# Performance work log

Measured on AMD Instinct MI355X. Metric: run time of the kernel, lower is better.

Reference implementation:

```python
import jax, jax.numpy as jnp
import numpy as np

N = 50000      # nodes
E = 800000     # edges (before self loops)
IN = 61        # input node features
H = 256        # hidden
HEADS = 8
C = H // HEADS # per-head channels = 32
L = 4          # GAT layers
EPS = 1e-5


def setup_inputs() -> dict:
    key = jax.random.key(0)
    ks = jax.random.split(key, 10)
    s = 0.05
    return {
        "x": jax.random.normal(ks[0], (N, IN), jnp.float32),
        "edge_index": jax.random.randint(ks[1], (2, E), 0, N),
        "in_W": jax.random.normal(ks[2], (IN, H), jnp.float32) * s,
        "in_b": jnp.zeros((H,), jnp.float32),
        "in_gamma": jnp.ones((H,), jnp.float32),
        "in_beta": jnp.zeros((H,), jnp.float32),
        "Ws": jax.random.normal(ks[3], (L, H, H), jnp.float32) * s,
        "att_src": jax.random.normal(ks[4], (L, HEADS, C), jnp.float32) * s,
        "att_dst": jax.random.normal(ks[5], (L, HEADS, C), jnp.float32) * s,
        "conv_b": jnp.zeros((L, H), jnp.float32),
        "bn_gamma": jnp.ones((L, H), jnp.float32),
        "bn_beta": jnp.zeros((L, H), jnp.float32),
        "mean_W": jax.random.normal(ks[6], (H, 1), jnp.float32) * s,
        "mean_b": jnp.zeros((1,), jnp.float32),
        "lv_W": jax.random.normal(ks[7], (H, 1), jnp.float32) * s,
        "lv_b": jnp.zeros((1,), jnp.float32),
    }


def _bn(h, gamma, beta):
    # training-mode BatchNorm1d: batch stats, biased variance
    mu = h.mean(axis=0)
    var = jnp.var(h, axis=0)
    return (h - mu) * jax.lax.rsqrt(var + EPS) * gamma + beta


def _gat_layer(h, src, dst, W, a_src, a_dst, bias):
    # h: [N,H] -> z: [N,HEADS,C]
    z = (h @ W).reshape(N, HEADS, C)
    e_src = jnp.einsum('nhc,hc->nh', z, a_src)  # [N,HEADS]
    e_dst = jnp.einsum('nhc,hc->nh', z, a_dst)
    e = jax.nn.leaky_relu(e_src[src] + e_dst[dst], 0.2)  # [Etot,HEADS]
    # segment softmax over destination neighborhoods
    emax = jax.ops.segment_max(e, dst, num_segments=N)
    p = jnp.exp(e - emax[dst])
    denom = jax.ops.segment_sum(p, dst, num_segments=N)
    alpha = p / denom[dst]
    # weighted scatter-aggregate of per-edge messages
    out = jax.ops.segment_sum(z[src] * alpha[:, :, None], dst, num_segments=N)
    return out.reshape(N, H) + bias


def reference(x, edge_index, in_W, in_b, in_gamma, in_beta, Ws, att_src,
              att_dst, conv_b, bn_gamma, bn_beta, mean_W, mean_b, lv_W, lv_b):
    loops = jnp.arange(N, dtype=edge_index.dtype)
    src = jnp.concatenate([edge_index[0], loops])  # add_self_loops=True
    dst = jnp.concatenate([edge_index[1], loops])
    # input projection: Linear -> BN -> ReLU (dropout off, deterministic)
    h = jax.nn.relu(_bn(x @ in_W + in_b, in_gamma, in_beta))
    for i in range(L):
        res = h
        h = _gat_layer(h, src, dst, Ws[i], att_src[i], att_dst[i], conv_b[i])
        h = jax.nn.relu(_bn(h, bn_gamma[i], bn_beta[i])) + res
    mean = (h @ mean_W + mean_b)[:, 0]
    log_var = jnp.clip((h @ lv_W + lv_b)[:, 0], -10.0, 10.0)
    return (mean, log_var)
```

## Files before the change

### kernel.cpp

```cpp
#include <hip/hip_runtime.h>
#include <hip/hip_fp16.h>

#define NN 50000
#define EE 800000
#define ETOT 850000
#define KIN 61
#define HH 256
#define NH 8
#define CC 32
#define LL 4
#define SCAN_NBLK 49

typedef __attribute__((ext_vector_type(8))) short bf16x8;
typedef __attribute__((ext_vector_type(4))) float f32x4;

__device__ __forceinline__ unsigned short f2b(float f) {
    unsigned u = __builtin_bit_cast(unsigned, f);
    u += 0x7fffu + ((u >> 16) & 1u);
    return (unsigned short)(u >> 16);
}
__device__ __forceinline__ float b2f(unsigned short h) {
    unsigned u = ((unsigned)h) << 16;
    return __builtin_bit_cast(float, u);
}
__device__ __forceinline__ unsigned short f2h(float f) {
    __half h = __float2half(f);
    return __builtin_bit_cast(unsigned short, h);
}
__device__ __forceinline__ float h2f(unsigned short u) {
    return __half2float(__builtin_bit_cast(__half, u));
}

__device__ __forceinline__ void gload16(const void* g, void* l) {
    __builtin_amdgcn_global_load_lds(
        (const __attribute__((address_space(1))) void*)g,
        (__attribute__((address_space(3))) void*)l, 16, 0, 0);
}


__global__ __launch_bounds__(256) void edge_hist(const int* __restrict__ ei,
                                                 int* __restrict__ counts) {
    int e = blockIdx.x * 256 + threadIdx.x;
    if (e >= ETOT) return;
    int d = (e < EE) ? ei[EE + e] : (e - EE);
    atomicAdd(&counts[d], 1);
}

__global__ __launch_bounds__(256) void scan1(const int* __restrict__ counts,
                                             int* __restrict__ tmp,
                                             int* __restrict__ bsums) {
    __shared__ int lds[256];
    int b = blockIdx.x, t = threadIdx.x;
    int base = b * 1024 + t * 4;
    int v0 = 0, v1 = 0, v2 = 0, v3 = 0;
    if (base + 0 < NN) v0 = counts[base + 0];
    if (base + 1 < NN) v1 = counts[base + 1];
    if (base + 2 < NN) v2 = counts[base + 2];
    if (base + 3 < NN) v3 = counts[base + 3];
    int s = v0 + v1 + v2 + v3;
    lds[t] = s;
    __syncthreads();
    for (int off = 1; off < 256; off <<= 1) {
        int x = (t >= off) ? lds[t - off] : 0;
        __syncthreads();
        lds[t] += x;
        __syncthreads();
    }
    int run = lds[t] - s;
    if (t == 255) bsums[b] = lds[255];
    run += v0; if (base + 0 < NN) tmp[base + 0] = run;
    run += v1; if (base + 1 < NN) tmp[base + 1] = run;
    run += v2; if (base + 2 < NN) tmp[base + 2] = run;
    run += v3; if (base + 3 < NN) tmp[base + 3] = run;
}

__global__ void scan2(int* __restrict__ bsums) {
    if (threadIdx.x == 0) {
        int acc = 0;
        for (int i = 0; i < SCAN_NBLK; ++i) { int t = bsums[i]; bsums[i] = acc; acc += t; }
    }
}

__global__ __launch_bounds__(256) void scan3(const int* __restrict__ tmp,
                                             const int* __restrict__ bsums,
                                             const int* __restrict__ counts,
                                             int* __restrict__ rowptr,
                                             int* __restrict__ cursor) {
    int i = blockIdx.x * 256 + threadIdx.x;
    if (i >= NN) return;
    int incl = tmp[i] + bsums[i >> 10];
    rowptr[i + 1] = incl;
    cursor[i] = incl - counts[i];
    if (i == 0) rowptr[0] = 0;
}

__global__ __launch_bounds__(256) void edge_scatter(const int* __restrict__ ei,
                                                    int* __restrict__ cursor,
                                                    int* __restrict__ ssrc) {
    int e = blockIdx.x * 256 + threadIdx.x;
    if (e >= ETOT) return;
    int s, d;
    if (e < EE) { s = ei[e]; d = ei[EE + e]; } else { s = d = e - EE; }
    int pos = atomicAdd(&cursor[d], 1);
    ssrc[pos] = s;
}

__global__ __launch_bounds__(256) void sort_rows(const int* __restrict__ rowptr,
                                                 int* __restrict__ ssrc) {
    int wid = (blockIdx.x * 256 + threadIdx.x) >> 6;
    int lane = threadIdx.x & 63;
    if (wid >= NN) return;
    int beg = rowptr[wid], end = rowptr[wid + 1];
    int L = end - beg;
    if (L > 64) return;
    int v = (lane < L) ? ssrc[beg + lane] : 0x7fffffff;
#pragma unroll
    for (int k = 2; k <= 64; k <<= 1) {
#pragma unroll
        for (int j = k >> 1; j > 0; j >>= 1) {
            int partner = __shfl_xor(v, j);
            bool up = ((lane & k) == 0);
            bool keepMin = (up == ((lane & j) == 0));
            int mn = min(v, partner), mx = max(v, partner);
            v = keepMin ? mn : mx;
        }
    }
    if (lane < L) ssrc[beg + lane] = v;
}


__global__ __launch_bounds__(256) void prep_wt(const float* __restrict__ Ws,
                                               unsigned short* __restrict__ WT) {
    int t = blockIdx.x * 256 + threadIdx.x;
    if (t >= LL * HH * HH) return;
    int l = t >> 16, rem = t & 65535;
    int n = rem >> 8, k = rem & 255;
    WT[t] = f2b(Ws[l * 65536 + k * HH + n]);
}

__global__ __launch_bounds__(256) void prep_inwt(const float* __restrict__ in_W,
                                                 unsigned short* __restrict__ WT) {
    int t = blockIdx.x * 256 + threadIdx.x;
    if (t >= HH * 64) return;
    int n = t >> 6, k = t & 63;
    WT[t] = (k < KIN) ? f2b(in_W[k * HH + n]) : 0;
}

__global__ __launch_bounds__(256) void prep_x(const float* __restrict__ x,
                                              unsigned short* __restrict__ xb) {
    int t = blockIdx.x * 256 + threadIdx.x;
    if (t >= NN * 64) return;
    int n = t >> 6, c = t & 63;
    xb[t] = (c < KIN) ? f2b(x[n * KIN + c]) : 0;
}

template<int ZHM>
__global__ __launch_bounds__(512) void gemm_mfma(const unsigned short* __restrict__ A,
                                                 const unsigned short* __restrict__ Bt,
                                                 unsigned short* __restrict__ C,
                                                 const float* __restrict__ asl,
                                                 const float* __restrict__ adl,
                                                 float* __restrict__ esrcT,
                                                 float* __restrict__ edstT,
                                                 int M, int K) {
    __shared__ unsigned short As[128 * 64];
    __shared__ unsigned short Bs[256 * 64];
    int row0 = blockIdx.x * 128;
    int tid = threadIdx.x;
    int w = tid >> 6, l = tid & 63;
    int wm = w >> 2, wn = w & 3;
    int r15 = l & 15, q = l >> 4;

    f32x4 acc[4][4] = {};

    int crow = l >> 3;
    int cs   = l & 7;

    for (int kt = 0; kt < K; kt += 64) {
        if (kt) __syncthreads();
#pragma unroll
        for (int c = 0; c < 2; ++c) {
            int r = w * 16 + c * 8 + crow;
            int sg = cs ^ (r & 7);
            int ga = row0 + r; if (ga >= M) ga = M - 1;
            gload16(&A[(size_t)ga * K + kt + sg * 8], &As[(w * 16 + c * 8) * 64]);
        }
#pragma unroll
        for (int c = 0; c < 4; ++c) {
            int r = w * 32 + c * 8 + crow;
            int sg = cs ^ (r & 7);
            gload16(&Bt[(size_t)r * K + kt + sg * 8], &Bs[(w * 32 + c * 8) * 64]);
        }
        __syncthreads();
#pragma unroll
        for (int kk = 0; kk < 2; ++kk) {
            bf16x8 aF[4], bF[4];
#pragma unroll
            for (int i = 0; i < 4; ++i) {
                int ar = wm * 64 + i * 16 + r15;
                aF[i] = *(bf16x8*)&As[ar * 64 + ((kk * 4 + q) ^ (ar & 7)) * 8];
                int br = wn * 64 + i * 16 + r15;
                bF[i] = *(bf16x8*)&Bs[br * 64 + ((kk * 4 + q) ^ (br & 7)) * 8];
            }
#pragma unroll
            for (int i = 0; i < 4; ++i)
#pragma unroll
                for (int j = 0; j < 4; ++j)
                    acc[i][j] = __builtin_amdgcn_mfma_f32_16x16x32_bf16(aF[i], bF[j], acc[i][j], 0, 0, 0);
        }
    }

#pragma unroll
    for (int i = 0; i < 4; ++i)
#pragma unroll
        for (int j = 0; j < 4; ++j) {
            int nc = wn * 64 + j * 16 + r15;
#pragma unroll
            for (int r = 0; r < 4; ++r) {
                int gr = row0 + wm * 64 + i * 16 + q * 4 + r;
                if (gr < M) {
                    if (ZHM)
                        C[(size_t)(nc >> 5) * NN * CC + (size_t)gr * CC + (nc & 31)] = f2h(acc[i][j][r]);
                    else
                        C[(size_t)gr * HH + nc] = f2b(acc[i][j][r]);
                }
            }
        }

    if constexpr (ZHM) {
        int hdbase = wn * 2;
        float as_[4], ad_[4];
#pragma unroll
        for (int j = 0; j < 4; ++j) {
            int idx = (hdbase + (j >> 1)) * CC + (j & 1) * 16 + r15;
            as_[j] = asl[idx];
            ad_[j] = adl[idx];
        }
#pragma unroll
        for (int h = 0; h < 2; ++h) {
#pragma unroll
            for (int i = 0; i < 4; ++i) {
                float pes[4], ped[4];
#pragma unroll
                for (int r = 0; r < 4; ++r) {
                    float v0 = h2f(f2h(acc[i][2 * h][r]));
                    float v1 = h2f(f2h(acc[i][2 * h + 1][r]));
                    pes[r] = v0 * as_[2 * h] + v1 * as_[2 * h + 1];
                    ped[r] = v0 * ad_[2 * h] + v1 * ad_[2 * h + 1];
                }
#pragma unroll
                for (int off = 1; off <= 8; off <<= 1) {
#pragma unroll
                    for (int r = 0; r < 4; ++r) {
                        pes[r] += __shfl_xor(pes[r], off);
                        ped[r] += __shfl_xor(ped[r], off);
                    }
                }
                int hd = hdbase + h;
                if (r15 < 8) {
                    int r = r15 & 3;
                    int gr = row0 + wm * 64 + i * 16 + q * 4 + r;
                    if (gr < M) {
                        if (r15 < 4) esrcT[(size_t)hd * NN + gr] = pes[r];
                        else         edstT[(size_t)hd * NN + gr] = ped[r];
                    }
                }
            }
        }
    }
}

#define MAXEB 2048
__global__ __launch_bounds__(256) void aggregate(const int* __restrict__ rowptr,
                                                 const int* __restrict__ ssrc,
                                                 const float* __restrict__ esrcT,
                                                 const float* __restrict__ edstT,
                                                 const unsigned short* __restrict__ zT,
                                                 unsigned short* __restrict__ outb,
                                                 float* __restrict__ sums) {
    __shared__ int   s_lds[MAXEB];
    __shared__ float p_lds[MAXEB];
    __shared__ int   rp_lds[33];
    __shared__ float ed_lds[32];
    __shared__ float ws1[4][8][4], ws2[4][8][4];
    int bid = blockIdx.x;
    int hd = bid & 7;
    int n0 = (bid >> 3) * 32;
    int tid = threadIdx.x;
    const float* esp = esrcT + (size_t)hd * NN;
    const unsigned short* zp = zT + (size_t)hd * NN * CC;

    if (tid <= 32) {
        int idx = n0 + tid;
        rp_lds[tid] = rowptr[idx > NN ? NN : idx];
    }
    if (tid < 32) {
        int nn = n0 + tid;
        ed_lds[tid] = (nn < NN) ? edstT[(size_t)hd * NN + nn] : 0.f;
    }
    __syncthreads();
    int beg0 = rp_lds[0];
    int total = rp_lds[32] - beg0;
    bool staged = (total <= MAXEB);
    if (staged) {
        for (int j = tid; j < total; j += 256) {
            int s = ssrc[beg0 + j];
            int jj = beg0 + j;
            int lo = 0, hi = 32;
#pragma unroll
            for (int st = 0; st < 5; ++st) {
                int mid = (lo + hi) >> 1;
                bool le = (rp_lds[mid] <= jj);
                lo = le ? mid : lo;
                hi = le ? hi : mid;
            }
            float e = esp[s] + ed_lds[lo];
            e = (e > 0.f) ? e : 0.2f * e;
            s_lds[j] = s;
            p_lds[j] = __expf(e);
        }
    }
    __syncthreads();

    int lane = tid & 63;
    int wv = tid >> 6;
    int g = lane >> 3;
    int nl = wv * 8 + g;
    int n = n0 + nl;
    int col = (lane & 7) * 4;
    bool act = n < NN;
    int jbeg = rp_lds[nl] - beg0;
    int jend = rp_lds[nl + 1] - beg0;

    float d0 = 0.f, d1 = 0.f, d2 = 0.f, d3 = 0.f;
    __half2 zero2 = __float2half2_rn(0.f);
    __half2 c0l = zero2, c0h = zero2, c1l = zero2, c1h = zero2;
    __half2 c2l = zero2, c2h = zero2, c3l = zero2, c3h = zero2;
    int j = jbeg;
    if (staged) {
        for (; j + 3 < jend; j += 4) {
            int s0 = s_lds[j], s1 = s_lds[j + 1], s2 = s_lds[j + 2], s3 = s_lds[j + 3];
            float p0 = p_lds[j], p1 = p_lds[j + 1], p2 = p_lds[j + 2], p3 = p_lds[j + 3];
            uint2 z0 = *(const uint2*)&zp[(size_t)(s0 * CC + col)];
            uint2 z1 = *(const uint2*)&zp[(size_t)(s1 * CC + col)];
            uint2 z2 = *(const uint2*)&zp[(size_t)(s2 * CC + col)];
            uint2 z3 = *(const uint2*)&zp[(size_t)(s3 * CC + col)];
            __half2 ph0 = __float2half2_rn(p0 * 0.0625f);
            __half2 ph1 = __float2half2_rn(p1 * 0.0625f);
            __half2 ph2 = __float2half2_rn(p2 * 0.0625f);
            __half2 ph3 = __float2half2_rn(p3 * 0.0625f);
            d0 += p0; d1 += p1; d2 += p2; d3 += p3;
            c0l = __hfma2(ph0, __builtin_bit_cast(__half2, z0.x), c0l);
            c0h = __hfma2(ph0, __builtin_bit_cast(__half2, z0.y), c0h);
            c1l = __hfma2(ph1, __builtin_bit_cast(__half2, z1.x), c1l);
            c1h = __hfma2(ph1, __builtin_bit_cast(__half2, z1.y), c1h);
            c2l = __hfma2(ph2, __builtin_bit_cast(__half2, z2.x), c2l);
            c2h = __hfma2(ph2, __builtin_bit_cast(__half2, z2.y), c2h);
            c3l = __hfma2(ph3, __builtin_bit_cast(__half2, z3.x), c3l);
            c3h = __hfma2(ph3, __builtin_bit_cast(__half2, z3.y), c3h);
        }
        for (; j < jend; ++j) {
            int s0 = s_lds[j];
            float p0 = p_lds[j];
            uint2 z0 = *(const uint2*)&zp[(size_t)(s0 * CC + col)];
            __half2 ph0 = __float2half2_rn(p0 * 0.0625f);
            d0 += p0;
            c0l = __hfma2(ph0, __builtin_bit_cast(__half2, z0.x), c0l);
            c0h = __hfma2(ph0, __builtin_bit_cast(__half2, z0.y), c0h);
        }
    } else {
        float ed = act ? ed_lds[nl] : 0.f;
        for (; j < jend; ++j) {
            int s0 = ssrc[beg0 + j];
            float es0 = esp[s0];
            uint2 z0 = *(const uint2*)&zp[(size_t)(s0 * CC + col)];
            float e0 = es0 + ed; e0 = (e0 > 0.f) ? e0 : 0.2f * e0;
            float p0 = __expf(e0);
            __half2 ph0 = __float2half2_rn(p0 * 0.0625f);
            d0 += p0;
            c0l = __hfma2(ph0, __builtin_bit_cast(__half2, z0.x), c0l);
            c0h = __hfma2(ph0, __builtin_bit_cast(__half2, z0.y), c0h);
        }
    }
    float v0 = 0.f, v1 = 0.f, v2 = 0.f, v3 = 0.f;
    if (act) {
        float den = (d0 + d1) + (d2 + d3);
        float inv = 16.f / den;
        float2 f0l = __half22float2(c0l), f1l = __half22float2(c1l);
        float2 f2l = __half22float2(c2l), f3l = __half22float2(c3l);
        float2 f0h = __half22float2(c0h), f1h = __half22float2(c1h);
        float2 f2h_ = __half22float2(c2h), f3h = __half22float2(c3h);
        ushort4 o;
        o.x = f2b(((f0l.x + f1l.x) + (f2l.x + f3l.x)) * inv);
        o.y = f2b(((f0l.y + f1l.y) + (f2l.y + f3l.y)) * inv);
        o.z = f2b(((f0h.x + f1h.x) + (f2h_.x + f3h.x)) * inv);
        o.w = f2b(((f0h.y + f1h.y) + (f2h_.y + f3h.y)) * inv);
        *(ushort4*)&outb[(size_t)n * HH + hd * CC + col] = o;
        v0 = b2f(o.x); v1 = b2f(o.y); v2 = b2f(o.z); v3 = b2f(o.w);
    }
    float q0 = v0 * v0, q1 = v1 * v1, q2 = v2 * v2, q3 = v3 * v3;
#pragma unroll
    for (int off = 8; off <= 32; off <<= 1) {
        v0 += __shfl_xor(v0, off); v1 += __shfl_xor(v1, off);
        v2 += __shfl_xor(v2, off); v3 += __shfl_xor(v3, off);
        q0 += __shfl_xor(q0, off); q1 += __shfl_xor(q1, off);
        q2 += __shfl_xor(q2, off); q3 += __shfl_xor(q3, off);
    }
    if (g == 0) {
        int slot = lane & 7;
        ws1[wv][slot][0] = v0; ws1[wv][slot][1] = v1;
        ws1[wv][slot][2] = v2; ws1[wv][slot][3] = v3;
        ws2[wv][slot][0] = q0; ws2[wv][slot][1] = q1;
        ws2[wv][slot][2] = q2; ws2[wv][slot][3] = q3;
    }
    __syncthreads();
    if (tid < 32) {
        int slot = tid & 7, k = tid >> 3;
        float s1v = ws1[0][slot][k] + ws1[1][slot][k] + ws1[2][slot][k] + ws1[3][slot][k];
        float s2v = ws2[0][slot][k] + ws2[1][slot][k] + ws2[2][slot][k] + ws2[3][slot][k];
        int ch = hd * CC + slot * 4 + k;
        atomicAdd(&sums[ch], s1v);
        atomicAdd(&sums[HH + ch], s2v);
    }
}

__global__ __launch_bounds__(256) void col_stats(const unsigned short* __restrict__ X,
                                                 float* __restrict__ sums) {
    int c = threadIdx.x;
    int rows_per_block = (NN + gridDim.x - 1) / gridDim.x;
    int r0 = blockIdx.x * rows_per_block;
    int r1 = min(NN, r0 + rows_per_block);
    float s = 0.f, q = 0.f;
    for (int r = r0; r < r1; ++r) {
        float v = b2f(X[(size_t)r * HH + c]);
        s += v; q += v * v;
    }
    atomicAdd(&sums[c], s);
    atomicAdd(&sums[HH + c], q);
}

__global__ __launch_bounds__(256) void bn_relu_add(const unsigned short* __restrict__ X,
                                                   const float* __restrict__ sums,
                                                   const float* __restrict__ gamma,
                                                   const float* __restrict__ beta,
                                                   const unsigned short* __restrict__ res,
                                                   unsigned short* __restrict__ outb) {
    int i = blockIdx.x * 256 + threadIdx.x;
    if (i >= NN * 64) return;
    int c4 = (i & 63) * 4;
    const float invN = 1.f / NN;
    ushort4 u = *(const ushort4*)(X + (size_t)i * 4);
    float v0 = b2f(u.x), v1 = b2f(u.y), v2 = b2f(u.z), v3 = b2f(u.w);
    float4 s1 = *(const float4*)&sums[c4];
    float4 s2 = *(const float4*)&sums[HH + c4];
    float4 gm = *(const float4*)&gamma[c4];
    float4 bt = *(const float4*)&beta[c4];
    float mn0 = s1.x * invN, mn1 = s1.y * invN, mn2 = s1.z * invN, mn3 = s1.w * invN;
    float rs0 = rsqrtf(fmaxf(s2.x * invN - mn0 * mn0, 0.f) + 1e-5f);
    float rs1 = rsqrtf(fmaxf(s2.y * invN - mn1 * mn1, 0.f) + 1e-5f);
    float rs2 = rsqrtf(fmaxf(s2.z * invN - mn2 * mn2, 0.f) + 1e-5f);
    float rs3 = rsqrtf(fmaxf(s2.w * invN - mn3 * mn3, 0.f) + 1e-5f);
    float r0 = fmaxf((v0 - mn0) * rs0 * gm.x + bt.x, 0.f);
    float r1 = fmaxf((v1 - mn1) * rs1 * gm.y + bt.y, 0.f);
    float r2 = fmaxf((v2 - mn2) * rs2 * gm.z + bt.z, 0.f);
    float r3 = fmaxf((v3 - mn3) * rs3 * gm.w + bt.w, 0.f);
    if (res) {
        ushort4 rv = *(const ushort4*)(res + (size_t)i * 4);
        r0 += b2f(rv.x); r1 += b2f(rv.y); r2 += b2f(rv.z); r3 += b2f(rv.w);
    }
    ushort4 ob;
    ob.x = f2b(r0); ob.y = f2b(r1); ob.z = f2b(r2); ob.w = f2b(r3);
    *(ushort4*)(outb + (size_t)i * 4) = ob;
}

__global__ __launch_bounds__(256) void out_proj(const unsigned short* __restrict__ h,
                                                const float* __restrict__ mW,
                                                const float* __restrict__ mb,
                                                const float* __restrict__ lW,
                                                const float* __restrict__ lb,
                                                float* __restrict__ out) {
    int wid = (blockIdx.x * 256 + threadIdx.x) >> 6;
    int lane = threadIdx.x & 63;
    if (wid >= NN) return;
    ushort4 hv = *(const ushort4*)&h[(size_t)wid * HH + lane * 4];
    float h0 = b2f(hv.x), h1 = b2f(hv.y), h2 = b2f(hv.z), h3 = b2f(hv.w);
    float4 wv = *(const float4*)&mW[lane * 4];
    float4 lv = *(const float4*)&lW[lane * 4];
    float sm = h0 * wv.x + h1 * wv.y + h2 * wv.z + h3 * wv.w;
    float sl = h0 * lv.x + h1 * lv.y + h2 * lv.z + h3 * lv.w;
    for (int off = 32; off > 0; off >>= 1) {
        sm += __shfl_down(sm, off);
        sl += __shfl_down(sl, off);
    }
    if (lane == 0) {
        out[wid] = sm + mb[0];
        float l = sl + lb[0];
        out[NN + wid] = fminf(10.f, fmaxf(-10.f, l));
    }
}

extern "C" void kernel_launch(void* const* d_in, const int* in_sizes, int n_in,
                              void* d_out, int out_size, void* d_ws, size_t ws_size,
                              hipStream_t stream) {
    const float* x        = (const float*)d_in[0];
    const int*   ei       = (const int*)d_in[1];
    const float* in_W     = (const float*)d_in[2];
    const float* in_gamma = (const float*)d_in[4];
    const float* in_beta  = (const float*)d_in[5];
    const float* Ws       = (const float*)d_in[6];
    const float* att_src  = (const float*)d_in[7];
    const float* att_dst  = (const float*)d_in[8];
    const float* bn_gamma = (const float*)d_in[10];
    const float* bn_beta  = (const float*)d_in[11];
    const float* mean_W   = (const float*)d_in[12];
    const float* mean_b   = (const float*)d_in[13];
    const float* lv_W     = (const float*)d_in[14];
    const float* lv_b     = (const float*)d_in[15];
    float* out = (float*)d_out;

    char* p = (char*)d_ws;
    unsigned short* z    = (unsigned short*)p; p += (size_t)NN * HH * 2;
    unsigned short* hb   = (unsigned short*)p; p += (size_t)NN * HH * 2;
    unsigned short* aggb = (unsigned short*)p; p += (size_t)NN * HH * 2;
    float* esrcT = (float*)p;                  p += (size_t)NN * NH * 4;
    float* edstT = (float*)p;                  p += (size_t)NN * NH * 4;
    float* sums = (float*)p;                   p += 512 * 4;
    unsigned short* WT   = (unsigned short*)p; p += (size_t)LL * HH * HH * 2;
    unsigned short* inWT = (unsigned short*)p; p += (size_t)HH * 64 * 2;
    int* counts = (int*)p;                     p += (size_t)NN * 4;
    int* rowptr = (int*)p;                     p += (size_t)(NN + 1) * 4;
    int* cursor = (int*)p;                     p += (size_t)NN * 4;
    int* ssrc   = (int*)p;                     p += (size_t)ETOT * 4;
    int* bsums  = (int*)p;                     p += 64 * 4;
    unsigned short* xb = aggb;

    hipMemsetAsync(counts, 0, NN * sizeof(int), stream);
    edge_hist<<<(ETOT + 255) / 256, 256, 0, stream>>>(ei, counts);
    scan1<<<SCAN_NBLK, 256, 0, stream>>>(counts, cursor, bsums);
    scan2<<<1, 64, 0, stream>>>(bsums);
    scan3<<<(NN + 255) / 256, 256, 0, stream>>>(cursor, bsums, counts, rowptr, cursor);
    edge_scatter<<<(ETOT + 255) / 256, 256, 0, stream>>>(ei, cursor, ssrc);
    sort_rows<<<(NN * 64 + 255) / 256, 256, 0, stream>>>(rowptr, ssrc);

    prep_wt<<<(LL * HH * HH + 255) / 256, 256, 0, stream>>>(Ws, WT);
    prep_inwt<<<(HH * 64 + 255) / 256, 256, 0, stream>>>(in_W, inWT);
    prep_x<<<(NN * 64 + 255) / 256, 256, 0, stream>>>(x, xb);

    gemm_mfma<0><<<(NN + 127) / 128, 512, 0, stream>>>(xb, inWT, z, nullptr, nullptr,
                                                       nullptr, nullptr, NN, 64);
    hipMemsetAsync(sums, 0, 512 * sizeof(float), stream);
    col_stats<<<1024, 256, 0, stream>>>(z, sums);
    bn_relu_add<<<(NN * 64 + 255) / 256, 256, 0, stream>>>(z, sums, in_gamma, in_beta,
                                                           nullptr, hb);

    for (int l = 0; l < LL; ++l) {
        const unsigned short* WTl = WT + (size_t)l * HH * HH;
        const float* asl = att_src + (size_t)l * NH * CC;
        const float* adl = att_dst + (size_t)l * NH * CC;
        const float* gl  = bn_gamma + (size_t)l * HH;
        const float* bl  = bn_beta + (size_t)l * HH;

        gemm_mfma<1><<<(NN + 127) / 128, 512, 0, stream>>>(hb, WTl, z, asl, adl,
                                                           esrcT, edstT, NN, HH);
        hipMemsetAsync(sums, 0, 512 * sizeof(float), stream);
        aggregate<<<((NN + 31) / 32) * 8, 256, 0, stream>>>(rowptr, ssrc, esrcT, edstT,
                                                            z, aggb, sums);
        bn_relu_add<<<(NN * 64 + 255) / 256, 256, 0, stream>>>(aggb, sums, gl, bl, hb, hb);
    }

    out_proj<<<(NN * 64 + 255) / 256, 256, 0, stream>>>(hb, mean_W, mean_b, lv_W, lv_b, out);
}
```

Baseline: 690.2 us.

## Fuse BatchNorm+ReLU+residual into GEMM A-load and final BN into output projection

Removes the standalone bn_relu_add kernels. Each layer's GEMM now computes the BN scale and shift from the column sums in shared memory. It applies BN, ReLU and the residual while staging the A tile, and writes the new hidden state as a side effect. The last layer's BN and residual are folded into the output-projection kernel. This saves a full read/write pass and a launch per layer, but the A tile is now loaded through registers with ALU work instead of async direct-to-LDS loads, which may slow the GEMM main loop.

```diff
diff --git a/kernel.cpp b/kernel.cpp
--- a/kernel.cpp
+++ b/kernel.cpp
@@ -26,9 +26,6 @@
 __device__ __forceinline__ unsigned short f2h(float f) {
     __half h = __float2half(f);
     return __builtin_bit_cast(unsigned short, h);
-}
-__device__ __forceinline__ float h2f(unsigned short u) {
-    return __half2float(__builtin_bit_cast(__half, u));
 }
 
 __device__ __forceinline__ void gload16(const void* g, void* l) {
@@ -154,23 +151,42 @@
     xb[t] = (c < KIN) ? f2b(x[n * KIN + c]) : 0;
 }
 
-template<int ZHM>
-__global__ __launch_bounds__(512) void gemm_mfma(const unsigned short* __restrict__ A,
+template<int MODE>
+__global__ __launch_bounds__(512) void gemm_mfma(const unsigned short* __restrict__ Asrc,
                                                  const unsigned short* __restrict__ Bt,
                                                  unsigned short* __restrict__ C,
                                                  const float* __restrict__ asl,
                                                  const float* __restrict__ adl,
                                                  float* __restrict__ esrcT,
                                                  float* __restrict__ edstT,
+                                                 const float* __restrict__ sums,
+                                                 const float* __restrict__ gamma,
+                                                 const float* __restrict__ beta,
+                                                 const unsigned short* __restrict__ res,
+                                                 unsigned short* __restrict__ hbNew,
                                                  int M, int K) {
     __shared__ unsigned short As[128 * 64];
     __shared__ unsigned short Bs[256 * 64];
+    __shared__ float scaleS[256], shiftS[256];
     int row0 = blockIdx.x * 128;
     int tid = threadIdx.x;
     int w = tid >> 6, l = tid & 63;
     int wm = w >> 2, wn = w & 3;
     int r15 = l & 15, q = l >> 4;
 
+    if constexpr (MODE == 1) {
+        if (tid < 256) {
+            const float invN = 1.f / NN;
+            float mn = sums[tid] * invN;
+            float var = fmaxf(sums[256 + tid] * invN - mn * mn, 0.f);
+            float rs = rsqrtf(var + 1e-5f);
+            float sc = rs * gamma[tid];
+            scaleS[tid] = sc;
+            shiftS[tid] = beta[tid] - mn * sc;
+        }
+        __syncthreads();
+    }
+
     f32x4 acc[4][4] = {};
 
     int crow = l >> 3;
@@ -182,8 +198,47 @@
         for (int c = 0; c < 2; ++c) {
             int r = w * 16 + c * 8 + crow;
             int sg = cs ^ (r & 7);
-            int ga = row0 + r; if (ga >= M) ga = M - 1;
-            gload16(&A[(size_t)ga * K + kt + sg * 8], &As[(w * 16 + c * 8) * 64]);
+            int ga = row0 + r;
+            if constexpr (MODE == 0) {
+                if (ga >= M) ga = M - 1;
+                gload16(&Asrc[(size_t)ga * K + kt + sg * 8], &As[(w * 16 + c * 8) * 64]);
+            } else {
+                unsigned short* dst = &As[(w * 16 + c * 8) * 64 + l * 8];
+                if (ga < M) {
+                    int ch = kt + sg * 8;
+                    ushort4 xlo = *(const ushort4*)&Asrc[(size_t)ga * 256 + ch];
+                    ushort4 xhi = *(const ushort4*)&Asrc[(size_t)ga * 256 + ch + 4];
+                    float4 sc0 = *(const float4*)&scaleS[ch];
+                    float4 sc1 = *(const float4*)&scaleS[ch + 4];
+                    float4 sh0 = *(const float4*)&shiftS[ch];
+                    float4 sh1 = *(const float4*)&shiftS[ch + 4];
+                    float f0 = fmaxf(b2f(xlo.x) * sc0.x + sh0.x, 0.f);
+                    float f1 = fmaxf(b2f(xlo.y) * sc0.y + sh0.y, 0.f);
+                    float f2 = fmaxf(b2f(xlo.z) * sc0.z + sh0.z, 0.f);
+                    float f3 = fmaxf(b2f(xlo.w) * sc0.w + sh0.w, 0.f);
+                    float f4 = fmaxf(b2f(xhi.x) * sc1.x + sh1.x, 0.f);
+                    float f5 = fmaxf(b2f(xhi.y) * sc1.y + sh1.y, 0.f);
+                    float f6 = fmaxf(b2f(xhi.z) * sc1.z + sh1.z, 0.f);
+                    float f7 = fmaxf(b2f(xhi.w) * sc1.w + sh1.w, 0.f);
+                    if (res) {
+                        ushort4 rlo = *(const ushort4*)&res[(size_t)ga * 256 + ch];
+                        ushort4 rhi = *(const ushort4*)&res[(size_t)ga * 256 + ch + 4];
+                        f0 += b2f(rlo.x); f1 += b2f(rlo.y); f2 += b2f(rlo.z); f3 += b2f(rlo.w);
+                        f4 += b2f(rhi.x); f5 += b2f(rhi.y); f6 += b2f(rhi.z); f7 += b2f(rhi.w);
+                    }
+                    ushort4 olo, ohi;
+                    olo.x = f2b(f0); olo.y = f2b(f1); olo.z = f2b(f2); olo.w = f2b(f3);
+                    ohi.x = f2b(f4); ohi.y = f2b(f5); ohi.z = f2b(f6); ohi.w = f2b(f7);
+                    *(ushort4*)dst = olo;
+                    *(ushort4*)(dst + 4) = ohi;
+                    *(ushort4*)&hbNew[(size_t)ga * 256 + ch] = olo;
+                    *(ushort4*)&hbNew[(size_t)ga * 256 + ch + 4] = ohi;
+                } else {
+                    ushort4 zz = {0, 0, 0, 0};
+                    *(ushort4*)dst = zz;
+                    *(ushort4*)(dst + 4) = zz;
+                }
+            }
         }
 #pragma unroll
         for (int c = 0; c < 4; ++c) {
@@ -219,7 +274,7 @@
             for (int r = 0; r < 4; ++r) {
                 int gr = row0 + wm * 64 + i * 16 + q * 4 + r;
                 if (gr < M) {
-                    if (ZHM)
+                    if (MODE == 1)
                         C[(size_t)(nc >> 5) * NN * CC + (size_t)gr * CC + (nc & 31)] = f2h(acc[i][j][r]);
                     else
                         C[(size_t)gr * HH + nc] = f2b(acc[i][j][r]);
@@ -227,7 +282,7 @@
             }
         }
 
-    if constexpr (ZHM) {
+    if constexpr (MODE == 1) {
         int hdbase = wn * 2;
         float as_[4], ad_[4];
 #pragma unroll
@@ -243,8 +298,8 @@
                 float pes[4], ped[4];
 #pragma unroll
                 for (int r = 0; r < 4; ++r) {
-                    float v0 = h2f(f2h(acc[i][2 * h][r]));
-                    float v1 = h2f(f2h(acc[i][2 * h + 1][r]));
+                    float v0 = __half2float(__float2half(acc[i][2 * h][r]));
+                    float v1 = __half2float(__float2half(acc[i][2 * h + 1][r]));
                     pes[r] = v0 * as_[2 * h] + v1 * as_[2 * h + 1];
                     ped[r] = v0 * ad_[2 * h] + v1 * ad_[2 * h + 1];
                 }
@@ -439,14 +494,19 @@
     atomicAdd(&sums[HH + c], q);
 }
 
-__global__ __launch_bounds__(256) void bn_relu_add(const unsigned short* __restrict__ X,
-                                                   const float* __restrict__ sums,
-                                                   const float* __restrict__ gamma,
-                                                   const float* __restrict__ beta,
-                                                   const unsigned short* __restrict__ res,
-                                                   unsigned short* __restrict__ outb) {
+__global__ __launch_bounds__(256) void bn_out(const unsigned short* __restrict__ X,
+                                              const float* __restrict__ sums,
+                                              const float* __restrict__ gamma,
+                                              const float* __restrict__ beta,
+                                              const unsigned short* __restrict__ res,
+                                              const float* __restrict__ mW,
+                                              const float* __restrict__ mb,
+                                              const float* __restrict__ lW,
+                                              const float* __restrict__ lb,
+                                              float* __restrict__ out) {
     int i = blockIdx.x * 256 + threadIdx.x;
-    if (i >= NN * 64) return;
+    int row = i >> 6;
+    int lane = threadIdx.x & 63;
     int c4 = (i & 63) * 4;
     const float invN = 1.f / NN;
     ushort4 u = *(const ushort4*)(X + (size_t)i * 4);
@@ -464,38 +524,20 @@
     float r1 = fmaxf((v1 - mn1) * rs1 * gm.y + bt.y, 0.f);
     float r2 = fmaxf((v2 - mn2) * rs2 * gm.z + bt.z, 0.f);
     float r3 = fmaxf((v3 - mn3) * rs3 * gm.w + bt.w, 0.f);
-    if (res) {
-        ushort4 rv = *(const ushort4*)(res + (size_t)i * 4);
-        r0 += b2f(rv.x); r1 += b2f(rv.y); r2 += b2f(rv.z); r3 += b2f(rv.w);
-    }
-    ushort4 ob;
-    ob.x = f2b(r0); ob.y = f2b(r1); ob.z = f2b(r2); ob.w = f2b(r3);
-    *(ushort4*)(outb + (size_t)i * 4) = ob;
-}
-
-__global__ __launch_bounds__(256) void out_proj(const unsigned short* __restrict__ h,
-                                                const float* __restrict__ mW,
-                                                const float* __restrict__ mb,
-                                                const float* __restrict__ lW,
-                                                const float* __restrict__ lb,
-                                                float* __restrict__ out) {
-    int wid = (blockIdx.x * 256 + threadIdx.x) >> 6;
-    int lane = threadIdx.x & 63;
-    if (wid >= NN) return;
-    ushort4 hv = *(const ushort4*)&h[(size_t)wid * HH + lane * 4];
-    float h0 = b2f(hv.x), h1 = b2f(hv.y), h2 = b2f(hv.z), h3 = b2f(hv.w);
-    float4 wv = *(const float4*)&mW[lane * 4];
-    float4 lv = *(const float4*)&lW[lane * 4];
-    float sm = h0 * wv.x + h1 * wv.y + h2 * wv.z + h3 * wv.w;
-    float sl = h0 * lv.x + h1 * lv.y + h2 * lv.z + h3 * lv.w;
+    ushort4 rv = *(const ushort4*)(res + (size_t)i * 4);
+    r0 += b2f(rv.x); r1 += b2f(rv.y); r2 += b2f(rv.z); r3 += b2f(rv.w);
+    float4 wv = *(const float4*)&mW[c4];
+    float4 lv = *(const float4*)&lW[c4];
+    float sm = r0 * wv.x + r1 * wv.y + r2 * wv.z + r3 * wv.w;
+    float sl = r0 * lv.x + r1 * lv.y + r2 * lv.z + r3 * lv.w;
     for (int off = 32; off > 0; off >>= 1) {
         sm += __shfl_down(sm, off);
         sl += __shfl_down(sl, off);
     }
     if (lane == 0) {
-        out[wid] = sm + mb[0];
-        float l = sl + lb[0];
-        out[NN + wid] = fminf(10.f, fmaxf(-10.f, l));
+        out[row] = sm + mb[0];
+        float l2 = sl + lb[0];
+        out[NN + row] = fminf(10.f, fmaxf(-10.f, l2));
     }
 }
 
@@ -546,27 +588,31 @@
     prep_inwt<<<(HH * 64 + 255) / 256, 256, 0, stream>>>(in_W, inWT);
     prep_x<<<(NN * 64 + 255) / 256, 256, 0, stream>>>(x, xb);
 
-    gemm_mfma<0><<<(NN + 127) / 128, 512, 0, stream>>>(xb, inWT, z, nullptr, nullptr,
-                                                       nullptr, nullptr, NN, 64);
+    gemm_mfma<0><<<(NN + 127) / 128, 512, 0, stream>>>(xb, inWT, hb, nullptr, nullptr,
+                                                       nullptr, nullptr, nullptr,
+                                                       nullptr, nullptr, nullptr,
+                                                       nullptr, NN, 64);
     hipMemsetAsync(sums, 0, 512 * sizeof(float), stream);
-    col_stats<<<1024, 256, 0, stream>>>(z, sums);
-    bn_relu_add<<<(NN * 64 + 255) / 256, 256, 0, stream>>>(z, sums, in_gamma, in_beta,
-                                                           nullptr, hb);
+    col_stats<<<1024, 256, 0, stream>>>(hb, sums);
 
     for (int l = 0; l < LL; ++l) {
         const unsigned short* WTl = WT + (size_t)l * HH * HH;
         const float* asl = att_src + (size_t)l * NH * CC;
         const float* adl = att_dst + (size_t)l * NH * CC;
-        const float* gl  = bn_gamma + (size_t)l * HH;
-        const float* bl  = bn_beta + (size_t)l * HH;
-
-        gemm_mfma<1><<<(NN + 127) / 128, 512, 0, stream>>>(hb, WTl, z, asl, adl,
-                                                           esrcT, edstT, NN, HH);
+        const unsigned short* bnX = (l == 0) ? hb : aggb;
+        const unsigned short* resp = (l == 0) ? nullptr : hb;
+        const float* gm = (l == 0) ? in_gamma : bn_gamma + (size_t)(l - 1) * HH;
+        const float* bt = (l == 0) ? in_beta  : bn_beta  + (size_t)(l - 1) * HH;
+
+        gemm_mfma<1><<<(NN + 127) / 128, 512, 0, stream>>>(bnX, WTl, z, asl, adl,
+                                                           esrcT, edstT, sums, gm, bt,
+                                                           resp, hb, NN, HH);
         hipMemsetAsync(sums, 0, 512 * sizeof(float), stream);
         aggregate<<<((NN + 31) / 32) * 8, 256, 0, stream>>>(rowptr, ssrc, esrcT, edstT,
                                                             z, aggb, sums);
-        bn_relu_add<<<(NN * 64 + 255) / 256, 256, 0, stream>>>(aggb, sums, gl, bl, hb, hb);
-    }
-
-    out_proj<<<(NN * 64 + 255) / 256, 256, 0, stream>>>(hb, mean_W, mean_b, lv_W, lv_b, out);
-}
+    }
+
+    bn_out<<<(NN * 64) / 256, 256, 0, stream>>>(aggb, sums, bn_gamma + 3 * HH,
+                                                bn_beta + 3 * HH, hb,
+                                                mean_W, mean_b, lv_W, lv_b, out);
+}
```

Result: faster. 656.4 us (-4.9%).
